# Kernel optimization log

Measured on AMD Instinct MI355X. Metric: run time of the kernel, lower is better.

Reference implementation:

```python
import jax, jax.numpy as jnp
import numpy as np

B, K, H_IMG, W_IMG = 8, 1, 512, 512
N_ITR = 10      # fixed iteration count (torch max_itr loop, unrolled via scan)
TOL = 1e-3      # convergence tolerance used for per-element gating


def setup_inputs() -> dict:
    key = jax.random.key(0)
    k1, k2 = jax.random.split(key)
    img = jax.random.normal(k1, (B, K, H_IMG, W_IMG), dtype=jnp.float32)
    temp = jax.random.normal(k2, (B, K, H_IMG, W_IMG), dtype=jnp.float32)
    return {"img": img, "temp": temp}


def _grad_batch(F):
    # central difference with replicate padding (== conv with [-0.5,0,0.5])
    px = jnp.pad(F, ((0, 0), (0, 0), (0, 0), (1, 1)), mode='edge')
    dx = 0.5 * (px[..., 2:] - px[..., :-2])
    py = jnp.pad(F, ((0, 0), (0, 0), (1, 1), (0, 0)), mode='edge')
    dy = 0.5 * (py[..., 2:, :] - py[..., :-2, :])
    return dx, dy


def _bilinear_sample(img, xp, yp):
    # img [B,k,h,w]; xp,yp pixel coords [B,h,w]; zeros padding, align_corners=True
    _, k, h, w = img.shape
    x0 = jnp.floor(xp)
    y0 = jnp.floor(yp)
    wx1 = xp - x0
    wy1 = yp - y0

    def tap(xi, yi, wgt):
        valid = (xi >= 0) & (xi <= w - 1) & (yi >= 0) & (yi <= h - 1)
        xc = jnp.clip(xi, 0, w - 1).astype(jnp.int32)
        yc = jnp.clip(yi, 0, h - 1).astype(jnp.int32)
        v = jax.vmap(lambda im, yy, xx: im[:, yy, xx])(img, yc, xc)  # [B,k,h,w]
        return v * (wgt * valid.astype(img.dtype))[:, None]

    return (tap(x0, y0, (1 - wx1) * (1 - wy1)) + tap(x0 + 1, y0, wx1 * (1 - wy1))
            + tap(x0, y0 + 1, (1 - wx1) * wy1) + tap(x0 + 1, y0 + 1, wx1 * wy1))


def _deeplk(img, temp):
    Bb, k, h, w = temp.shape
    gx, gy = _grad_batch(temp)
    # centered pixel coordinates (meshgrid with x - x.max()/2)
    xs = jnp.arange(w, dtype=jnp.float32) - (w - 1) / 2.0
    ys = jnp.arange(h, dtype=jnp.float32) - (h - 1) / 2.0
    X, Y = jnp.meshgrid(xs, ys)  # each [h,w]
    Xf = jnp.tile(X.reshape(-1), k)  # [k*h*w]
    Yf = jnp.tile(Y.reshape(-1), k)
    gxf = gx.reshape(Bb, -1)
    gyf = gy.reshape(Bb, -1)
    # Jacobian dI/dp: [B, k*h*w, 8]
    dIdp = jnp.stack([
        Xf * gxf, Yf * gxf, gxf,
        Xf * gyf, Yf * gyf, gyf,
        -Xf * Xf * gxf - Xf * Yf * gyf,
        -Xf * Yf * gxf - Yf * Yf * gyf], axis=-1)
    Hm = jnp.einsum('bni,bnj->bij', dIdp, dIdp)        # [B,8,8]
    invH = jnp.linalg.inv(Hm)
    invH_dIdp = jnp.einsum('bij,bnj->bin', invH, dIdp)  # [B,8,N]

    xy1 = jnp.stack([X.reshape(-1), Y.reshape(-1),
                     jnp.ones(h * w, jnp.float32)], axis=0)  # [3, h*w]
    I3 = jnp.eye(3, dtype=jnp.float32)

    def param_to_H(p):
        return I3 + jnp.concatenate([p, jnp.zeros((Bb, 1), p.dtype)], 1).reshape(Bb, 3, 3)

    def step(carry, _):
        p, dp = carry  # p,dp: [B,8]
        Hh = param_to_H(p)
        xyw = jnp.einsum('bij,jn->bin', Hh, xy1)
        Xw = (xyw[:, 0] / xyw[:, 2]).reshape(Bb, h, w) + (w - 1) / 2.0
        Yw = (xyw[:, 1] / xyw[:, 2]).reshape(Bb, h, w) + (h - 1) / 2.0
        Fi_warp = _bilinear_sample(img, Xw, Yw)
        xn = Xw / ((w - 1) / 2.0) - 1.0
        yn = Yw / ((h - 1) / 2.0) - 1.0
        mask = ((xn > -1 + 2.0 / w) & (xn < 1 - 2.0 / w) &
                (yn > -1 + 2.0 / h) & (yn < 1 - 2.0 / h)).astype(img.dtype)
        r = (Fi_warp - temp * mask[:, None]).reshape(Bb, -1)  # [B,N]
        dp_new = jnp.einsum('bin,bn->bi', invH_dIdp, r)       # [B,8]
        dp_new = dp_new.at[:, 6:8].set(0.0)                   # no projective update
        gate = (jnp.linalg.norm(dp, axis=1, keepdims=True) > TOL).astype(p.dtype)
        dp_next = gate * dp_new
        return (p - dp_next, dp_next), None

    p0 = jnp.zeros((Bb, 8), jnp.float32)
    dp0 = jnp.ones((Bb, 8), jnp.float32)
    (p, _), _ = jax.lax.scan(step, (p0, dp0), None, length=N_ITR)
    return p.reshape(Bb, 8, 1), param_to_H(p)


def reference(img, temp):
    return _deeplk(img, temp)
```

## Files before the change

### kernel.cpp

```cpp
#include <hip/hip_runtime.h>
#include <math.h>

#define W     512
#define HH    512
#define NB    8
#define NBLK  512
#define TPB   512
#define NW    (TPB / 64)
#define BPB   64
#define ROWS  8
#define NPX   (ROWS * W)
#define PXT   (NPX / TPB)
#define NITR  10
#define POISON64 0xAAAAAAAAAAAAAAAAull
#define ALL64  0xFFFFFFFFFFFFFFFFull
#define MLO 0.998046875f
#define MHI 510.001953125f

__device__ __forceinline__ float wave_reduce64(float x) {
    x += __shfl_down(x, 32, 64);
    x += __shfl_down(x, 16, 64);
    x += __shfl_down(x, 8, 64);
    x += __shfl_down(x, 4, 64);
    x += __shfl_down(x, 2, 64);
    x += __shfl_down(x, 1, 64);
    return x;
}
__device__ __forceinline__ double load_d(const double* p) {
    unsigned long long u = __hip_atomic_load((const unsigned long long*)p,
                       __ATOMIC_RELAXED, __HIP_MEMORY_SCOPE_AGENT);
    return __builtin_bit_cast(double, u);
}
__device__ __forceinline__ void store_d(double* p, double v) {
    __hip_atomic_store((unsigned long long*)p, __builtin_bit_cast(unsigned long long, v),
                       __ATOMIC_RELAXED, __HIP_MEMORY_SCOPE_AGENT);
}
__device__ __forceinline__ bool not_poison(double v) {
    return __builtin_bit_cast(unsigned long long, v) != POISON64;
}

__device__ __forceinline__ float hrec(int t, float X1, float X2, float X3, float X4,
    float a0, float a1, float a2, float b0, float b1, float b2, float b3,
    float c0, float c1, float c2, float c3, float c4)
{
    switch (t) {
    case 0:  return X2 * a0;             case 1:  return X1 * a1;
    case 2:  return X1 * a0;             case 3:  return X2 * b0;
    case 4:  return X1 * b1;             case 5:  return X1 * b0;
    case 6:  return -(X3 * a0 + X2 * b1);
    case 7:  return -(X2 * a1 + X1 * b2);
    case 8:  return a2;                  case 9:  return a1;
    case 10: return X1 * b1;             case 11: return b2;
    case 12: return b1;
    case 13: return -(X2 * a1 + X1 * b2);
    case 14: return -(X1 * a2 + b3);
    case 15: return a0;                  case 16: return X1 * b0;
    case 17: return b1;                  case 18: return b0;
    case 19: return -(X2 * a0 + X1 * b1);
    case 20: return -(X1 * a1 + b2);
    case 21: return X2 * c0;             case 22: return X1 * c1;
    case 23: return X1 * c0;
    case 24: return -(X3 * b0 + X2 * c1);
    case 25: return -(X2 * b1 + X1 * c2);
    case 26: return c2;                  case 27: return c1;
    case 28: return -(X2 * b1 + X1 * c2);
    case 29: return -(X1 * b2 + c3);
    case 30: return c0;
    case 31: return -(X2 * b0 + X1 * c1);
    case 32: return -(X1 * b1 + c2);
    case 33: return X4 * a0 + 2.f * X3 * b1 + X2 * c2;
    case 34: return X3 * a1 + 2.f * X2 * b2 + X1 * c3;
    default: return X2 * a2 + 2.f * X1 * b3 + c4;
    }
}

extern "C" __global__ __launch_bounds__(TPB, 4)
void deeplk_kernel(const float* __restrict__ img, const float* __restrict__ temp,
                   float* __restrict__ out, void* __restrict__ wsv)
{
    double* Hpart = (double*)wsv;
    double* vpart = Hpart + NB * 36 * BPB;

    const int tid   = threadIdx.x;
    const int lane  = tid & 63;
    const int wv    = tid >> 6;
    const int b     = blockIdx.x & 7;
    const int chunk = blockIdx.x >> 3;
    const int row0  = chunk * ROWS;
    const float* tb = temp + b * (HH * W);
    const float* ib = img  + b * (HH * W);

    __shared__ float  s_gx[NPX], s_gy[NPX], s_tv[NPX];
    __shared__ double s_Hu[36];
    __shared__ double s_invH[64];
    __shared__ double s_p[8], s_dp[8], s_v[8];
    __shared__ float  s_wred[NW * 9];
    __shared__ double s_vred[NW * 8];

    const float X1 = (float)tid - 255.5f;

#pragma unroll
    for (int u = 0; u < PXT; ++u) {
        const int i  = tid + u * TPB;
        const int rr = row0 + u;
        const int cc = tid;
        const int cl = (cc > 0) ? cc - 1 : 0;
        const int cr = (cc < W - 1) ? cc + 1 : W - 1;
        const int ru = (rr > 0) ? rr - 1 : 0;
        const int rd = (rr < HH - 1) ? rr + 1 : HH - 1;
        s_gx[i] = 0.5f * (tb[rr * W + cr] - tb[rr * W + cl]);
        s_gy[i] = 0.5f * (tb[rd * W + cc] - tb[ru * W + cc]);
        s_tv[i] = tb[rr * W + cc];
    }
    __syncthreads();

    float a0 = 0.f, a1 = 0.f, a2 = 0.f;
    float b0 = 0.f, b1 = 0.f, b2 = 0.f, b3 = 0.f;
    float c0 = 0.f, c1 = 0.f, c2 = 0.f, c3 = 0.f, c4 = 0.f;
    {
        float Yv = (float)row0 - 255.5f;
#pragma unroll
        for (int u = 0; u < PXT; ++u) {
            const int i = tid + u * TPB;
            const float gx = s_gx[i], gy = s_gy[i];
            const float q1 = gx * gx, q2 = gx * gy, q3 = gy * gy;
            const float y2 = Yv * Yv, y3 = y2 * Yv, y4 = y2 * y2;
            a0 += q1; a1 += Yv * q1; a2 += y2 * q1;
            b0 += q2; b1 += Yv * q2; b2 += y2 * q2; b3 += y3 * q2;
            c0 += q3; c1 += Yv * q3; c2 += y2 * q3; c3 += y3 * q3; c4 += y4 * q3;
            Yv += 1.f;
        }
    }
    {
        const float X2 = X1 * X1, X3 = X2 * X1, X4 = X2 * X2;
#pragma unroll
        for (int grp = 0; grp < 4; ++grp) {
#pragma unroll
            for (int k = 0; k < 9; ++k) {
                float x = wave_reduce64(hrec(grp * 9 + k, X1, X2, X3, X4,
                                             a0, a1, a2, b0, b1, b2, b3,
                                             c0, c1, c2, c3, c4));
                if (lane == 0) s_wred[wv * 9 + k] = x;
            }
            __syncthreads();
            if (tid < 9) {
                double s = 0.0;
#pragma unroll
                for (int w2 = 0; w2 < NW; ++w2) s += (double)s_wred[w2 * 9 + tid];
                store_d(&Hpart[(b * 36 + grp * 9 + tid) * BPB + chunk], s);
            }
            __syncthreads();
        }
    }
    for (int c = wv; c < 36; c += NW) {
        const double* hp = &Hpart[(b * 36 + c) * BPB + lane];
        double x;
        for (;;) {
            x = load_d(hp);
            if (__ballot(not_poison(x)) == ALL64) break;
            __builtin_amdgcn_s_sleep(1);
        }
        x += __shfl_down(x, 32, 64);
        x += __shfl_down(x, 16, 64);
        x += __shfl_down(x, 8, 64);
        x += __shfl_down(x, 4, 64);
        x += __shfl_down(x, 2, 64);
        x += __shfl_down(x, 1, 64);
        if (lane == 0) s_Hu[c] = x;
    }
    __syncthreads();

    if (tid < 64) {
        const int r  = tid >> 3, cj = tid & 7;
        const int i2 = (r < cj) ? r : cj;
        const int j2 = (r < cj) ? cj : r;
        double a = s_Hu[i2 * 8 - (i2 * (i2 - 1)) / 2 + (j2 - i2)];
        double e = (r == cj) ? 1.0 : 0.0;
#pragma unroll
        for (int k = 0; k < 8; ++k) {
            int pr = k;
            double pv = fabs(__shfl(a, k * 8 + k, 64));
            for (int rr2 = k + 1; rr2 < 8; ++rr2) {
                double c = fabs(__shfl(a, rr2 * 8 + k, 64));
                if (c > pv) { pv = c; pr = rr2; }
            }
            double a_k = __shfl(a, k * 8 + cj, 64),  e_k = __shfl(e, k * 8 + cj, 64);
            double a_p = __shfl(a, pr * 8 + cj, 64), e_p = __shfl(e, pr * 8 + cj, 64);
            if (r == k)       { a = a_p; e = e_p; }
            else if (r == pr) { a = a_k; e = e_k; }
            double piv = __shfl(a, k * 8 + k, 64);
            double d = 1.0 / piv;
            if (r == k) { a *= d; e *= d; }
            double f  = __shfl(a, r * 8 + k, 64);
            double ak = __shfl(a, k * 8 + cj, 64);
            double ek = __shfl(e, k * 8 + cj, 64);
            if (r != k) { a -= f * ak; e -= f * ek; }
        }
        s_invH[tid] = e;
    }
    if (tid < 8) { s_p[tid] = 0.0; s_dp[tid] = 1.0; }
    __syncthreads();

    for (int it = 0; it < NITR; ++it) {
        double n2 = 0.0;
#pragma unroll
        for (int l = 0; l < 8; ++l) { double d = s_dp[l]; n2 += d * d; }
        if (n2 > 1e-6) {
            const float a00 = 1.f + (float)s_p[0];
            const float a01 = (float)s_p[1];
            const float a02 = (float)s_p[2] + 255.5f;
            const float a10 = (float)s_p[3];
            const float a11 = 1.f + (float)s_p[4];
            const float a12 = (float)s_p[5] + 255.5f;
            float Yv = (float)row0 - 255.5f;
            float Xw = a00 * X1 + a01 * Yv + a02;
            float Yw = a10 * X1 + a11 * Yv + a12;
            float A = 0.f, Bv = 0.f, Cv = 0.f, Dv = 0.f, Ev = 0.f;

#pragma unroll
            for (int u = 0; u < PXT; ++u) {
                const int i = tid + u * TPB;
                const float xf = floorf(Xw), yf = floorf(Yw);
                const int ix = (int)xf, iy = (int)yf;
                const float wx = Xw - xf, wy = Yw - yf;
                const bool vx0 = (ix >= 0) & (ix < W);
                const bool vx1 = (ix >= -1) & (ix < W - 1);
                const bool vy0 = (iy >= 0) & (iy < HH);
                const bool vy1 = (iy >= -1) & (iy < HH - 1);
                const float* ro0 = ib + iy * W;
                const float* ro1 = ro0 + W;
                const float t00 = (vx0 && vy0) ? ro0[ix]     : 0.f;
                const float t10 = (vx1 && vy0) ? ro0[ix + 1] : 0.f;
                const float t01 = (vx0 && vy1) ? ro1[ix]     : 0.f;
                const float t11 = (vx1 && vy1) ? ro1[ix + 1] : 0.f;
                const float omx = 1.f - wx, omy = 1.f - wy;
                const float Fi = (t00 * omx + t10 * wx) * omy
                               + (t01 * omx + t11 * wx) * wy;
                const float m = (Xw > MLO && Xw < MHI && Yw > MLO && Yw < MHI) ? 1.f : 0.f;
                const float rv = Fi - s_tv[i] * m;
                const float t1 = s_gx[i] * rv, t2 = s_gy[i] * rv;
                A  += t1;        Bv += t2;
                Cv += Yv * t1;   Dv += Yv * t2;
                Ev += (Yv * Yv) * t2;
                Xw += a01; Yw += a11; Yv += 1.f;
            }
            float va[8];
            {
                const float X2 = X1 * X1;
                va[0] = X1 * A;  va[1] = Cv;  va[2] = A;
                va[3] = X1 * Bv; va[4] = Dv;  va[5] = Bv;
                va[6] = -(X2 * A + X1 * Dv);
                va[7] = -(X1 * Cv + Ev);
            }
#pragma unroll
            for (int c = 0; c < 8; ++c) {
                float x = wave_reduce64(va[c]);
                if (lane == 0) s_wred[wv * 8 + c] = x;
            }
            __syncthreads();
            double* vp = vpart + ((it * NB) + b) * BPB * 8;
            if (tid < 8) {
                double s = 0.0;
#pragma unroll
                for (int w2 = 0; w2 < NW; ++w2) s += (double)s_wred[w2 * 8 + tid];
                store_d(&vp[chunk * 8 + tid], s);
            }
            {
                const double* slot = &vp[tid];
                double x;
                for (;;) {
                    x = load_d(slot);
                    if (__ballot(not_poison(x)) == ALL64) break;
                    __builtin_amdgcn_s_sleep(1);
                }
                x += __shfl_down(x, 32, 64);
                x += __shfl_down(x, 16, 64);
                x += __shfl_down(x, 8, 64);
                if (lane < 8) s_vred[wv * 8 + lane] = x;
            }
            __syncthreads();
            if (tid < 8) {
                double s = 0.0;
#pragma unroll
                for (int w2 = 0; w2 < NW; ++w2) s += s_vred[w2 * 8 + tid];
                s_v[tid] = s;
            }
            __syncthreads();
            if (tid < 8) {
                double dpn = 0.0;
#pragma unroll
                for (int l = 0; l < 8; ++l) dpn += s_invH[tid * 8 + l] * s_v[l];
                if (tid >= 6) dpn = 0.0;
                s_p[tid] -= dpn;
                s_dp[tid] = dpn;
            }
            __syncthreads();
        }
    }

    if (chunk == 0) {
        if (tid < 8) out[b * 8 + tid] = (float)s_p[tid];
        if (tid == 0) {
            float* Ho = out + 64 + b * 9;
            Ho[0] = 1.f + (float)s_p[0]; Ho[1] = (float)s_p[1];       Ho[2] = (float)s_p[2];
            Ho[3] = (float)s_p[3];       Ho[4] = 1.f + (float)s_p[4]; Ho[5] = (float)s_p[5];
            Ho[6] = (float)s_p[6];       Ho[7] = (float)s_p[7];       Ho[8] = 1.f;
        }
    }
}

extern "C" void kernel_launch(void* const* d_in, const int* in_sizes, int n_in,
                              void* d_out, int out_size, void* d_ws, size_t ws_size,
                              hipStream_t stream) {
    const float* img  = (const float*)d_in[0];
    const float* temp = (const float*)d_in[1];
    float* out = (float*)d_out;
    void*  ws  = d_ws;
    void* args[] = { &img, &temp, &out, &ws };
    hipError_t e = hipLaunchCooperativeKernel((const void*)deeplk_kernel, dim3(NBLK),
                                              dim3(TPB), args, 0, stream);
    if (e != hipSuccess) {
        deeplk_kernel<<<dim3(NBLK), dim3(TPB), 0, stream>>>(img, temp, out, ws);
    }
}
```

Baseline: 164.7 us.

## Fuse first Lucas-Kanade iteration into Hessian accumulation pass

At p=0 the warp is the identity, so the first iteration's residual is computed with direct image reads during the Hessian/gradient pass, skipping bilinear sampling. Its partial sums are reduced through the same cross-block slot exchange as the Hessian, and the first dp is formed right after the matrix inverse. The iteration loop then starts at 1, which removes one full grid-wide synchronisation round and one sampling pass. The mask and the vpart slot reuse (iteration 0 slots) must match the original semantics exactly.

```diff
diff --git a/kernel.cpp b/kernel.cpp
--- a/kernel.cpp
+++ b/kernel.cpp
@@ -117,17 +117,26 @@
     float a0 = 0.f, a1 = 0.f, a2 = 0.f;
     float b0 = 0.f, b1 = 0.f, b2 = 0.f, b3 = 0.f;
     float c0 = 0.f, c1 = 0.f, c2 = 0.f, c3 = 0.f, c4 = 0.f;
+    float A = 0.f, Bv = 0.f, Cv = 0.f, Dv = 0.f, Ev = 0.f;
     {
+        const bool xm = (tid >= 1) && (tid <= 510);
         float Yv = (float)row0 - 255.5f;
 #pragma unroll
         for (int u = 0; u < PXT; ++u) {
-            const int i = tid + u * TPB;
+            const int i  = tid + u * TPB;
+            const int rr = row0 + u;
             const float gx = s_gx[i], gy = s_gy[i];
             const float q1 = gx * gx, q2 = gx * gy, q3 = gy * gy;
             const float y2 = Yv * Yv, y3 = y2 * Yv, y4 = y2 * y2;
             a0 += q1; a1 += Yv * q1; a2 += y2 * q1;
             b0 += q2; b1 += Yv * q2; b2 += y2 * q2; b3 += y3 * q2;
             c0 += q3; c1 += Yv * q3; c2 += y2 * q3; c3 += y3 * q3; c4 += y4 * q3;
+            const float m  = (xm && rr >= 1 && rr <= 510) ? 1.f : 0.f;
+            const float rv = ib[rr * W + tid] - s_tv[i] * m;
+            const float t1 = gx * rv, t2 = gy * rv;
+            A  += t1;        Bv += t2;
+            Cv += Yv * t1;   Dv += Yv * t2;
+            Ev += y2 * t2;
             Yv += 1.f;
         }
     }
@@ -150,6 +159,23 @@
                 store_d(&Hpart[(b * 36 + grp * 9 + tid) * BPB + chunk], s);
             }
             __syncthreads();
+        }
+        float va[8];
+        va[0] = X1 * A;  va[1] = Cv;  va[2] = A;
+        va[3] = X1 * Bv; va[4] = Dv;  va[5] = Bv;
+        va[6] = -(X2 * A + X1 * Dv);
+        va[7] = -(X1 * Cv + Ev);
+#pragma unroll
+        for (int c = 0; c < 8; ++c) {
+            float x = wave_reduce64(va[c]);
+            if (lane == 0) s_wred[wv * 9 + c] = x;
+        }
+        __syncthreads();
+        if (tid < 8) {
+            double s = 0.0;
+#pragma unroll
+            for (int w2 = 0; w2 < NW; ++w2) s += (double)s_wred[w2 * 9 + tid];
+            store_d(&vpart[b * BPB * 8 + chunk * 8 + tid], s);
         }
     }
     for (int c = wv; c < 36; c += NW) {
@@ -167,6 +193,26 @@
         x += __shfl_down(x, 2, 64);
         x += __shfl_down(x, 1, 64);
         if (lane == 0) s_Hu[c] = x;
+    }
+    {
+        const double* slot = &vpart[b * BPB * 8 + tid];
+        double x;
+        for (;;) {
+            x = load_d(slot);
+            if (__ballot(not_poison(x)) == ALL64) break;
+            __builtin_amdgcn_s_sleep(1);
+        }
+        x += __shfl_down(x, 32, 64);
+        x += __shfl_down(x, 16, 64);
+        x += __shfl_down(x, 8, 64);
+        if (lane < 8) s_vred[wv * 8 + lane] = x;
+    }
+    __syncthreads();
+    if (tid < 8) {
+        double s = 0.0;
+#pragma unroll
+        for (int w2 = 0; w2 < NW; ++w2) s += s_vred[w2 * 8 + tid];
+        s_v[tid] = s;
     }
     __syncthreads();
 
@@ -198,10 +244,18 @@
         }
         s_invH[tid] = e;
     }
-    if (tid < 8) { s_p[tid] = 0.0; s_dp[tid] = 1.0; }
-    __syncthreads();
-
-    for (int it = 0; it < NITR; ++it) {
+    __syncthreads();
+    if (tid < 8) {
+        double dpn = 0.0;
+#pragma unroll
+        for (int l = 0; l < 8; ++l) dpn += s_invH[tid * 8 + l] * s_v[l];
+        if (tid >= 6) dpn = 0.0;
+        s_p[tid]  = -dpn;
+        s_dp[tid] = dpn;
+    }
+    __syncthreads();
+
+    for (int it = 1; it < NITR; ++it) {
         double n2 = 0.0;
 #pragma unroll
         for (int l = 0; l < 8; ++l) { double d = s_dp[l]; n2 += d * d; }
@@ -215,7 +269,7 @@
             float Yv = (float)row0 - 255.5f;
             float Xw = a00 * X1 + a01 * Yv + a02;
             float Yw = a10 * X1 + a11 * Yv + a12;
-            float A = 0.f, Bv = 0.f, Cv = 0.f, Dv = 0.f, Ev = 0.f;
+            float Ai = 0.f, Bi = 0.f, Ci = 0.f, Di = 0.f, Ei = 0.f;
 
 #pragma unroll
             for (int u = 0; u < PXT; ++u) {
@@ -239,30 +293,30 @@
                 const float m = (Xw > MLO && Xw < MHI && Yw > MLO && Yw < MHI) ? 1.f : 0.f;
                 const float rv = Fi - s_tv[i] * m;
                 const float t1 = s_gx[i] * rv, t2 = s_gy[i] * rv;
-                A  += t1;        Bv += t2;
-                Cv += Yv * t1;   Dv += Yv * t2;
-                Ev += (Yv * Yv) * t2;
+                Ai += t1;        Bi += t2;
+                Ci += Yv * t1;   Di += Yv * t2;
+                Ei += (Yv * Yv) * t2;
                 Xw += a01; Yw += a11; Yv += 1.f;
             }
             float va[8];
             {
                 const float X2 = X1 * X1;
-                va[0] = X1 * A;  va[1] = Cv;  va[2] = A;
-                va[3] = X1 * Bv; va[4] = Dv;  va[5] = Bv;
-                va[6] = -(X2 * A + X1 * Dv);
-                va[7] = -(X1 * Cv + Ev);
+                va[0] = X1 * Ai; va[1] = Ci;  va[2] = Ai;
+                va[3] = X1 * Bi; va[4] = Di;  va[5] = Bi;
+                va[6] = -(X2 * Ai + X1 * Di);
+                va[7] = -(X1 * Ci + Ei);
             }
 #pragma unroll
             for (int c = 0; c < 8; ++c) {
                 float x = wave_reduce64(va[c]);
-                if (lane == 0) s_wred[wv * 8 + c] = x;
+                if (lane == 0) s_wred[wv * 9 + c] = x;
             }
             __syncthreads();
             double* vp = vpart + ((it * NB) + b) * BPB * 8;
             if (tid < 8) {
                 double s = 0.0;
 #pragma unroll
-                for (int w2 = 0; w2 < NW; ++w2) s += (double)s_wred[w2 * 8 + tid];
+                for (int w2 = 0; w2 < NW; ++w2) s += (double)s_wred[w2 * 9 + tid];
                 store_d(&vp[chunk * 8 + tid], s);
             }
             {
```

Result: no change. 162.4 us (-1.3%).
